# Kernel tuning notes

Hardware: AMD Instinct MI355X
Metric: run time of the kernel (lower is better)

Reference implementation:

```python
import jax, jax.numpy as jnp
import numpy as np

MAX_TRAV = 21  # matches the torch module constant


def setup_inputs() -> dict:
    key = jax.random.key(0)
    k1, _ = jax.random.split(key)
    B, H, W = 4, 2048, 2048
    untraversable = jax.random.randint(k1, (B, H, W), 0, 2).astype(jnp.bool_)
    max_sq = jnp.ones((1,), dtype=jnp.float32) * float(MAX_TRAV ** 2)  # 441.0
    return {"untraversable": untraversable, "max_sq": max_sq}


def _chamfer(untraversable, max_sq):
    big = max_sq[0]
    B, H, W = untraversable.shape
    # 0 at obstacles, MAX_TRAV^2 elsewhere (values are small exact ints in fp32)
    sq = jnp.where(untraversable, jnp.float32(0.0), big)
    # odd increments 1,3,...,41: cumulative sum of first k odds = k^2
    ds = jnp.arange(1, 2 * MAX_TRAV + 1, 2, dtype=jnp.float32)

    col = jnp.full((B, H, 1), big, dtype=jnp.float32)

    def hstep(s, d):
        from_right = jnp.concatenate([s[:, :, 1:] + d, col], axis=2)
        from_left = jnp.concatenate([col, s[:, :, :-1] + d], axis=2)
        return jnp.minimum(s, jnp.minimum(from_right, from_left)), None

    sq, _ = jax.lax.scan(hstep, sq, ds)

    row = jnp.full((B, 1, W), big, dtype=jnp.float32)

    def vstep(s, d):
        from_below = jnp.concatenate([s[:, 1:, :] + d, row], axis=1)
        from_above = jnp.concatenate([row, s[:, :-1, :] + d], axis=1)
        return jnp.minimum(s, jnp.minimum(from_below, from_above)), None

    sq, _ = jax.lax.scan(vstep, sq, ds)
    return jnp.sqrt(sq)


def reference(untraversable, max_sq):
    return _chamfer(untraversable, max_sq)
```

## Files before the change

kernel.cpp:

```cpp
#include <hip/hip_runtime.h>
#include <cstdint>

#define BB 4
#define HH 2048
#define WW 2048
#define MAXT 21
#define BIGSQ 441

static __device__ __forceinline__ uint32_t umin32(uint32_t a, uint32_t b) { return a < b ? a : b; }

__global__ __launch_bounds__(256) void hpass(const int* __restrict__ in,
                                             uint8_t* __restrict__ dh) {
    const int tid  = threadIdx.x;
    const int lane = tid & 63;
    const int w    = tid >> 6;
    const int row  = blockIdx.x;
    const long long ro = (long long)row * WW;
    const int x0   = w << 9;

    int v[8];
    #pragma unroll
    for (int j = 0; j < 8; ++j)
        v[j] = in[ro + x0 + (j << 6) + lane];

    unsigned long long b[10];
    b[0] = 0; b[9] = 0;
    if (x0 > 0)
        b[0] = __ballot(in[ro + x0 - 64 + lane] != 0);
    if (x0 + 512 < WW)
        b[9] = __ballot(in[ro + x0 + 512 + lane] != 0);
    #pragma unroll
    for (int j = 0; j < 8; ++j)
        b[j + 1] = __ballot(v[j] != 0);

    #pragma unroll
    for (int j = 0; j < 8; ++j) {
        const unsigned long long mc = b[j + 1];
        unsigned long long right = mc >> lane;
        if (lane) right |= b[j + 2] << (64 - lane);
        unsigned long long left = mc << (63 - lane);
        if (lane != 63) left |= b[j] >> (lane + 1);

        int dr = right ? __builtin_ctzll(right) : 64;
        int dl = left  ? __builtin_clzll(left)  : 64;
        int d  = min(min(dr, dl), MAXT);
        dh[ro + x0 + (j << 6) + lane] = (uint8_t)d;
    }
}

__global__ __launch_bounds__(256) void vpass(const uint8_t* __restrict__ dh,
                                             float* __restrict__ out) {
    __shared__ uint16_t s[106][128];
    const int tid = threadIdx.x;
    const int x0  = blockIdx.x << 7;
    const int y0  = blockIdx.y << 6;
    const int b   = blockIdx.z;
    const long long base = (long long)b * HH * WW;

    for (int i = tid; i < 106 * 16; i += 256) {
        int r  = i >> 4;
        int c8 = (i & 15) << 3;
        int gy = y0 - 21 + r;
        uint4 pk;
        if (gy >= 0 && gy < HH) {
            const uint8_t* p = dh + base + (long long)gy * WW + x0 + c8;
            uint2 u = *(const uint2*)p;
            uint32_t e0 = u.x & 0xff, e1 = (u.x >> 8) & 0xff, e2 = (u.x >> 16) & 0xff, e3 = u.x >> 24;
            uint32_t e4 = u.y & 0xff, e5 = (u.y >> 8) & 0xff, e6 = (u.y >> 16) & 0xff, e7 = u.y >> 24;
            pk.x = (e0 * e0) | ((e1 * e1) << 16);
            pk.y = (e2 * e2) | ((e3 * e3) << 16);
            pk.z = (e4 * e4) | ((e5 * e5) << 16);
            pk.w = (e6 * e6) | ((e7 * e7) << 16);
        } else {
            pk.x = pk.y = pk.z = pk.w = BIGSQ | (BIGSQ << 16);
        }
        *(uint4*)&s[r][c8] = pk;
    }
    __syncthreads();

    const int lane = tid & 63;
    const int w    = tid >> 6;
    const int cg   = (lane & 31) << 2;
    const int ro   = lane >> 5;
    for (int k = 0; k < 8; ++k) {
        const int j  = (w << 4) + (k << 1) + ro;
        const int yl = 21 + j;

        uint2 q = *(const uint2*)&s[yl][cg];
        uint32_t v0 = q.x & 0xffff, v1 = q.x >> 16;
        uint32_t v2 = q.y & 0xffff, v3 = q.y >> 16;

        for (int d = 1; d <= MAXT; ++d) {
            const uint32_t dd = (uint32_t)(d * d);
            uint32_t h = umin32(0, 0);
            h = v0 > v1 ? v0 : v1;
            uint32_t h2 = v2 > v3 ? v2 : v3;
            h = h > h2 ? h : h2;
            if (__all(dd >= h)) break;
            uint2 a  = *(const uint2*)&s[yl - d][cg];
            uint2 bq = *(const uint2*)&s[yl + d][cg];
            const uint32_t dd2 = dd * 0x10001u;
            uint32_t A0 = a.x + dd2, A1 = a.y + dd2;
            uint32_t B0 = bq.x + dd2, B1 = bq.y + dd2;
            v0 = umin32(v0, umin32(A0 & 0xffff, B0 & 0xffff));
            v1 = umin32(v1, umin32(A0 >> 16,    B0 >> 16));
            v2 = umin32(v2, umin32(A1 & 0xffff, B1 & 0xffff));
            v3 = umin32(v3, umin32(A1 >> 16,    B1 >> 16));
        }

        float4 o;
        o.x = sqrtf((float)v0);
        o.y = sqrtf((float)v1);
        o.z = sqrtf((float)v2);
        o.w = sqrtf((float)v3);
        *(float4*)&out[base + (long long)(y0 + j) * WW + x0 + cg] = o;
    }
}

extern "C" void kernel_launch(void* const* d_in, const int* in_sizes, int n_in,
                              void* d_out, int out_size, void* d_ws, size_t ws_size,
                              hipStream_t stream) {
    const int* unt = (const int*)d_in[0];
    uint8_t* dh    = (uint8_t*)d_ws;
    float* out     = (float*)d_out;

    hpass<<<dim3(BB * HH), 256, 0, stream>>>(unt, dh);
    vpass<<<dim3(WW / 128, HH / 64, BB), 256, 0, stream>>>(dh, out);
}
```

Baseline: 41.46 us.

## Process one row per wavefront in hpass with vectorized pair loads

The horizontal pass now gives each wavefront a whole row and walks it in 16 chunks. Each lane loads two adjacent ints as a uint2 and stores two distance bytes as one 16-bit write. Even and odd columns are tracked in separate ballots, and bit reversal plus a sentinel-bounded 32-bit ctz computes left and right distances, which removes the halo reloads and cuts the store count. Launch bounds ask for 4 blocks per CU. In exchange, the 16 uint2 values held per lane raise register pressure, and the interleaved-parity bit logic is complex and error-prone.

New measurement: 40.97 us. About the same (-1.2%).

```diff
diff --git a/kernel.cpp b/kernel.cpp
--- a/kernel.cpp
+++ b/kernel.cpp
@@ -9,42 +9,58 @@
 
 static __device__ __forceinline__ uint32_t umin32(uint32_t a, uint32_t b) { return a < b ? a : b; }
 
-__global__ __launch_bounds__(256) void hpass(const int* __restrict__ in,
-                                             uint8_t* __restrict__ dh) {
+__global__ __launch_bounds__(256, 4) void hpass(const int* __restrict__ in,
+                                                uint8_t* __restrict__ dh) {
     const int tid  = threadIdx.x;
     const int lane = tid & 63;
     const int w    = tid >> 6;
-    const int row  = blockIdx.x;
+    const int row  = (blockIdx.x << 2) + w;
     const long long ro = (long long)row * WW;
-    const int x0   = w << 9;
+    const int* rp = in + ro;
+    const int li = 63 - lane;
 
-    int v[8];
+    uint2 u[16];
     #pragma unroll
-    for (int j = 0; j < 8; ++j)
-        v[j] = in[ro + x0 + (j << 6) + lane];
+    for (int c = 0; c < 16; ++c)
+        u[c] = *(const uint2*)(rp + (c << 7) + (lane << 1));
 
-    unsigned long long b[10];
-    b[0] = 0; b[9] = 0;
-    if (x0 > 0)
-        b[0] = __ballot(in[ro + x0 - 64 + lane] != 0);
-    if (x0 + 512 < WW)
-        b[9] = __ballot(in[ro + x0 + 512 + lane] != 0);
-    #pragma unroll
-    for (int j = 0; j < 8; ++j)
-        b[j + 1] = __ballot(v[j] != 0);
+    unsigned long long b0p = 0, b1p = 0;
+    unsigned long long b0c = __ballot(u[0].x != 0);
+    unsigned long long b1c = __ballot(u[0].y != 0);
 
     #pragma unroll
-    for (int j = 0; j < 8; ++j) {
-        const unsigned long long mc = b[j + 1];
-        unsigned long long right = mc >> lane;
-        if (lane) right |= b[j + 2] << (64 - lane);
-        unsigned long long left = mc << (63 - lane);
-        if (lane != 63) left |= b[j] >> (lane + 1);
+    for (int c = 0; c < 16; ++c) {
+        unsigned long long b0n = 0, b1n = 0;
+        if (c < 15) {
+            b0n = __ballot(u[c + 1].x != 0);
+            b1n = __ballot(u[c + 1].y != 0);
+        }
+        unsigned long long rb0c = __brevll(b1c), rb1c = __brevll(b0c);
+        unsigned long long rb0p = __brevll(b1p), rb1p = __brevll(b0p);
 
-        int dr = right ? __builtin_ctzll(right) : 64;
-        int dl = left  ? __builtin_clzll(left)  : 64;
-        int d  = min(min(dr, dl), MAXT);
-        dh[ro + x0 + (j << 6) + lane] = (uint8_t)d;
+        unsigned long long S0  = (b0c >> lane) | ((b0n << 1) << li);
+        unsigned long long S1  = (b1c >> lane) | ((b1n << 1) << li);
+        unsigned long long SL0 = (rb0c >> li)  | ((rb0p << 1) << lane);
+        unsigned long long SL1 = (rb1c >> li)  | ((rb1p << 1) << lane);
+
+        const uint32_t SEN = 1u << 11;
+        uint32_t s0 = (uint32_t)S0, s1 = (uint32_t)S1;
+        uint32_t l0 = (uint32_t)SL0, l1 = (uint32_t)SL1;
+        int t_s0  = __builtin_ctz(s0 | SEN);
+        int t_s1  = __builtin_ctz(s1 | SEN);
+        int t_s0s = __builtin_ctz((s0 >> 1) | SEN);
+        int t_l0  = __builtin_ctz(l0 | SEN);
+        int t_l1  = __builtin_ctz(l1 | SEN);
+        int t_l0s = __builtin_ctz((l0 >> 1) | SEN);
+
+        int d0 = min(min(2 * t_s0, 2 * t_s1 + 1), min(2 * t_l1, 2 * t_l0s + 1));
+        int d1 = min(min(2 * t_s1, 2 * t_s0s + 1), min(2 * t_l0, 2 * t_l1 + 1));
+        d0 = min(d0, MAXT);
+        d1 = min(d1, MAXT);
+
+        *(uint16_t*)(dh + ro + (c << 7) + (lane << 1)) = (uint16_t)(d0 | (d1 << 8));
+
+        b0p = b0c; b1p = b1c; b0c = b0n; b1c = b1n;
     }
 }
 
@@ -64,9 +80,9 @@
         uint4 pk;
         if (gy >= 0 && gy < HH) {
             const uint8_t* p = dh + base + (long long)gy * WW + x0 + c8;
-            uint2 u = *(const uint2*)p;
-            uint32_t e0 = u.x & 0xff, e1 = (u.x >> 8) & 0xff, e2 = (u.x >> 16) & 0xff, e3 = u.x >> 24;
-            uint32_t e4 = u.y & 0xff, e5 = (u.y >> 8) & 0xff, e6 = (u.y >> 16) & 0xff, e7 = u.y >> 24;
+            uint2 uu = *(const uint2*)p;
+            uint32_t e0 = uu.x & 0xff, e1 = (uu.x >> 8) & 0xff, e2 = (uu.x >> 16) & 0xff, e3 = uu.x >> 24;
+            uint32_t e4 = uu.y & 0xff, e5 = (uu.y >> 8) & 0xff, e6 = (uu.y >> 16) & 0xff, e7 = uu.y >> 24;
             pk.x = (e0 * e0) | ((e1 * e1) << 16);
             pk.y = (e2 * e2) | ((e3 * e3) << 16);
             pk.z = (e4 * e4) | ((e5 * e5) << 16);
@@ -92,8 +108,7 @@
 
         for (int d = 1; d <= MAXT; ++d) {
             const uint32_t dd = (uint32_t)(d * d);
-            uint32_t h = umin32(0, 0);
-            h = v0 > v1 ? v0 : v1;
+            uint32_t h  = v0 > v1 ? v0 : v1;
             uint32_t h2 = v2 > v3 ? v2 : v3;
             h = h > h2 ? h : h2;
             if (__all(dd >= h)) break;
@@ -124,6 +139,6 @@
     uint8_t* dh    = (uint8_t*)d_ws;
     float* out     = (float*)d_out;
 
-    hpass<<<dim3(BB * HH), 256, 0, stream>>>(unt, dh);
+    hpass<<<dim3(BB * HH / 4), 256, 0, stream>>>(unt, dh);
     vpass<<<dim3(WW / 128, HH / 64, BB), 256, 0, stream>>>(dh, out);
 }
```
